# Optimization experiments

Hardware: AMD Instinct MI355X
Metric: run time of the kernel (lower is better)

## Reference

```python
import jax, jax.numpy as jnp
import numpy as np
import math

N_HEADS = 4
GROUPS = 32
EPS = 1e-5


def group_norm(x, w, b, groups=GROUPS):
    B, C, H, W = x.shape
    xg = x.reshape(B, groups, C // groups, H, W)
    mu = xg.mean(axis=(2, 3, 4), keepdims=True)
    var = xg.var(axis=(2, 3, 4), keepdims=True)
    xn = ((xg - mu) / jnp.sqrt(var + EPS)).reshape(B, C, H, W)
    return xn * w[None, :, None, None] + b[None, :, None, None]


def setup_inputs() -> dict:
    key = jax.random.key(0)
    ks = jax.random.split(key, 8)
    B, C, H, W = 4, 256, 64, 64
    s = 1.0 / math.sqrt(C)
    return {
        "x": jax.random.normal(ks[0], (B, C, H, W), jnp.float32),
        "context": jax.random.normal(ks[1], (B, C, H, W), jnp.float32),
        "gn_q_w": jnp.ones((C,), jnp.float32),
        "gn_q_b": jnp.zeros((C,), jnp.float32),
        "gn_ctx_w": jnp.ones((C,), jnp.float32),
        "gn_ctx_b": jnp.zeros((C,), jnp.float32),
        "Wq": jax.random.normal(ks[2], (C, C), jnp.float32) * s,
        "Wk": jax.random.normal(ks[3], (C, C), jnp.float32) * s,
        "Wv": jax.random.normal(ks[4], (C, C), jnp.float32) * s,
        "Wo": jax.random.normal(ks[5], (C, C), jnp.float32) * s,
        "bo": jnp.zeros((C,), jnp.float32),
    }


def reference(x, context, gn_q_w, gn_q_b, gn_ctx_w, gn_ctx_b, Wq, Wk, Wv, Wo, bo):
    B, C, H, W = x.shape
    hd = C // N_HEADS
    # 1x1 convs == channel matmuls
    q = jnp.einsum('oc,bchw->bohw', Wq, group_norm(x, gn_q_w, gn_q_b))
    k = jnp.einsum('oc,bchw->bohw', Wk, group_norm(context, gn_ctx_w, gn_ctx_b))
    v = jnp.einsum('oc,bchw->bohw', Wv, context)
    q = q.reshape(B, N_HEADS, hd, H * W)
    k = k.reshape(B, N_HEADS, hd, H * W)
    v = v.reshape(B, N_HEADS, hd, H * W)
    attn = jnp.einsum('bncd,bnce->bnde', q, k) / math.sqrt(hd)  # [B,n,HW,HW]
    attn = jax.nn.softmax(attn, axis=-1)
    out = jnp.einsum('bnde,bnce->bncd', attn, v).reshape(B, C, H, W)
    out = jnp.einsum('oc,bchw->bohw', Wo, out) + bo[None, :, None, None]
    return x + out
```

## Files before the change

kernel.cpp:

```cpp
#include <hip/hip_runtime.h>

typedef __bf16 bf16x8 __attribute__((ext_vector_type(8)));
typedef __bf16 bf16x2 __attribute__((ext_vector_type(2)));
typedef float f32x2 __attribute__((ext_vector_type(2)));
typedef float f32x4 __attribute__((ext_vector_type(4)));
typedef float f32x16 __attribute__((ext_vector_type(16)));

#define DEV static __device__ __forceinline__

DEV unsigned short f2bf(float f) {
  union { float f; unsigned int u; } v; v.f = f;
  unsigned int u = v.u;
  return (unsigned short)((u + 0x7FFFu + ((u >> 16) & 1u)) >> 16);
}

DEV float bf2f(unsigned short s) {
  union { unsigned u; float f; } v; v.u = ((unsigned)s) << 16; return v.f;
}

DEV bf16x8 ldb8(const unsigned short* p) { return *reinterpret_cast<const bf16x8*>(p); }

DEV bf16x8 ldsb8(const unsigned short* base, int byteoff) {
  return *reinterpret_cast<const bf16x8*>((const char*)base + byteoff);
}

DEV f32x4 mfma(bf16x8 a, bf16x8 b, f32x4 c) {
  return __builtin_amdgcn_mfma_f32_16x16x32_bf16(a, b, c, 0, 0, 0);
}
DEV f32x16 mfma32(bf16x8 a, bf16x8 b, f32x16 c) {
  return __builtin_amdgcn_mfma_f32_32x32x16_bf16(a, b, c, 0, 0, 0);
}

DEV float fexp2(float x) {
  float r;
  asm("v_exp_f32 %0, %1" : "=v"(r) : "v"(x));
  return r;
}

DEV unsigned cvtpk(float a, float b) {
  f32x2 t = {a, b};
  bf16x2 r = __builtin_convertvector(t, bf16x2);
  return __builtin_bit_cast(unsigned, r);
}

DEV bf16x8 pack4(unsigned w0, unsigned w1, unsigned w2, unsigned w3) {
  union { unsigned u[4]; bf16x8 v; } x;
  x.u[0] = w0; x.u[1] = w1; x.u[2] = w2; x.u[3] = w3;
  return x.v;
}

DEV f32x16 zero16() {
  f32x16 z;
#pragma unroll
  for (int i = 0; i < 16; ++i) z[i] = 0.f;
  return z;
}

__global__ __launch_bounds__(256) void gn_stats_kernel(
    const float* __restrict__ x, const float* __restrict__ ctx,
    const float* __restrict__ gqw, const float* __restrict__ gqb,
    const float* __restrict__ gcw, const float* __restrict__ gcb,
    float* __restrict__ ssbuf) {
  int id = blockIdx.x;
  int tensor = id >> 7;
  int bg = id & 127;
  int b = bg >> 5, g = bg & 31;
  const float* src = tensor ? ctx : x;
  const float* gw = tensor ? gcw : gqw;
  const float* gb = tensor ? gcb : gqb;
  float* scale = ssbuf + tensor * 2048;
  float* shift = scale + 1024;

  const float* base = src + (size_t)(b * 256 + g * 8) * 4096;
  int tid = threadIdx.x;
  float s = 0.f, sq = 0.f;
#pragma unroll
  for (int i = 0; i < 32; ++i) {
    float4 v = *reinterpret_cast<const float4*>(base + (i * 256 + tid) * 4);
    s += v.x + v.y + v.z + v.w;
    sq += v.x * v.x + v.y * v.y + v.z * v.z + v.w * v.w;
  }
#pragma unroll
  for (int sh = 32; sh; sh >>= 1) {
    s += __shfl_down(s, sh);
    sq += __shfl_down(sq, sh);
  }
  __shared__ float rs[4], rq[4], mr[2];
  int w = tid >> 6;
  if ((tid & 63) == 0) { rs[w] = s; rq[w] = sq; }
  __syncthreads();
  if (tid == 0) {
    float S = rs[0] + rs[1] + rs[2] + rs[3];
    float Q = rq[0] + rq[1] + rq[2] + rq[3];
    float mean = S * (1.f / 32768.f);
    float var = Q * (1.f / 32768.f) - mean * mean;
    mr[0] = mean;
    mr[1] = rsqrtf(var + 1e-5f);
  }
  __syncthreads();
  if (tid < 8) {
    int c = g * 8 + tid;
    float sc = gw[c] * mr[1];
    scale[b * 256 + c] = sc;
    shift[b * 256 + c] = gb[c] - mr[0] * sc;
  }
}

template <int OUTMODE>
__global__ __launch_bounds__(256) void proj_kernel(
    const float* __restrict__ W, const float* __restrict__ in,
    const float* __restrict__ scale, const float* __restrict__ shift,
    unsigned short* __restrict__ out, float wscale) {
  __shared__ unsigned short Alds[128][72];
  __shared__ unsigned short Blds[128][72];
  const int b = blockIdx.z;
  const int o0 = blockIdx.y * 128;
  const int p0 = blockIdx.x * 128;
  const int tid = threadIdx.x;
  const int w = tid >> 6, lane = tid & 63;
  const int g = lane >> 4, l15 = lane & 15;
  const int oh = (w >> 1) * 64, ph = (w & 1) * 64;

  f32x4 acc[4][4];
#pragma unroll
  for (int i = 0; i < 4; ++i)
#pragma unroll
    for (int j = 0; j < 4; ++j) acc[i][j] = (f32x4){0.f, 0.f, 0.f, 0.f};

  for (int kk = 0; kk < 4; ++kk) {
    const int c0 = kk * 64;
    __syncthreads();
#pragma unroll
    for (int i = 0; i < 8; ++i) {
      int idx = i * 256 + tid;
      int row = idx >> 4, col4 = (idx & 15) * 4;
      float4 wv = *reinterpret_cast<const float4*>(&W[(size_t)(o0 + row) * 256 + c0 + col4]);
      ushort4 bv = {f2bf(wv.x * wscale), f2bf(wv.y * wscale),
                    f2bf(wv.z * wscale), f2bf(wv.w * wscale)};
      *reinterpret_cast<ushort4*>(&Alds[row][col4]) = bv;
    }
#pragma unroll
    for (int i = 0; i < 8; ++i) {
      int idx = i * 256 + tid;
      int cc = idx >> 5, p4 = (idx & 31) * 4;
      int c = c0 + cc;
      float4 xv = *reinterpret_cast<const float4*>(&in[((size_t)b * 256 + c) * 4096 + p0 + p4]);
      float sc = 1.f, sh = 0.f;
      if (scale) { sc = scale[b * 256 + c]; sh = shift[b * 256 + c]; }
      Blds[p4 + 0][cc] = f2bf(xv.x * sc + sh);
      Blds[p4 + 1][cc] = f2bf(xv.y * sc + sh);
      Blds[p4 + 2][cc] = f2bf(xv.z * sc + sh);
      Blds[p4 + 3][cc] = f2bf(xv.w * sc + sh);
    }
    __syncthreads();
#pragma unroll
    for (int kf = 0; kf < 2; ++kf) {
      bf16x8 av[4], bv[4];
#pragma unroll
      for (int mf = 0; mf < 4; ++mf) av[mf] = ldb8(&Alds[oh + mf * 16 + l15][kf * 32 + g * 8]);
#pragma unroll
      for (int nf = 0; nf < 4; ++nf) bv[nf] = ldb8(&Blds[ph + nf * 16 + l15][kf * 32 + g * 8]);
#pragma unroll
      for (int mf = 0; mf < 4; ++mf)
#pragma unroll
        for (int nf = 0; nf < 4; ++nf) acc[mf][nf] = mfma(av[mf], bv[nf], acc[mf][nf]);
    }
  }
#pragma unroll
  for (int mf = 0; mf < 4; ++mf)
#pragma unroll
    for (int nf = 0; nf < 4; ++nf) {
      int o = o0 + oh + mf * 16 + g * 4;
      int p = p0 + ph + nf * 16 + l15;
      if (OUTMODE == 0) {
        int h = o >> 6, ch = o & 63;
        ushort4 vv = {f2bf(acc[mf][nf][0]), f2bf(acc[mf][nf][1]),
                      f2bf(acc[mf][nf][2]), f2bf(acc[mf][nf][3])};
        *reinterpret_cast<ushort4*>(&out[(((size_t)b * 4 + h) * 4096 + p) * 64 + ch]) = vv;
      } else {
#pragma unroll
        for (int r = 0; r < 4; ++r) {
          int oo = o + r;
          out[(((size_t)b * 4 + (oo >> 6)) * 64 + (oo & 63)) * 4096 + p] = f2bf(acc[mf][nf][r]);
        }
      }
    }
}

DEV void stageK32(const unsigned short* kg, int e0, char* ldsbase, int tidg) {
  int o = tidg * 16;
  int r = o >> 7;
  int col = (o & 127) ^ ((r & 7) << 4);
  const char* src = (const char*)(kg + (size_t)(e0 + r) * 64) + col;
  __builtin_amdgcn_global_load_lds(
      (__attribute__((address_space(1))) void*)src,
      (__attribute__((address_space(3))) void*)(ldsbase + (tidg >> 6) * 1024), 16, 0, 0);
}

DEV void stageV32(const unsigned short* vg, int e0, char* ldsbase, int tidg) {
  int o = tidg * 16;
  int c = o >> 6;
  int slotL = ((o >> 4) & 3) ^ ((c >> 1) & 3);
  const char* src = (const char*)(vg + (size_t)c * 4096 + e0 + slotL * 8);
  __builtin_amdgcn_global_load_lds(
      (__attribute__((address_space(1))) void*)src,
      (__attribute__((address_space(3))) void*)(ldsbase + (tidg >> 6) * 1024), 16, 0, 0);
}

__global__ __launch_bounds__(512) void attn_kernel(
    const unsigned short* __restrict__ QT, const unsigned short* __restrict__ KT,
    const unsigned short* __restrict__ V, unsigned short* __restrict__ OP,
    float* __restrict__ LP) {
  __shared__ __align__(16) char smem[34816];
  const int bh = blockIdx.x;
  const int split = blockIdx.z;
  const int tid = threadIdx.x;
  const int w = tid >> 6, lane = tid & 63;
  const int g = w >> 2, wl = w & 3;
  const int tidg = tid & 255;
  const int hi = lane >> 5, l31 = lane & 31;
  const int d = blockIdx.y * 128 + wl * 32 + l31;

  char* Kb0 = smem + g * 16384;
  char* Kb1 = Kb0 + 4096;
  char* Vb0 = Kb0 + 8192;
  char* Vb1 = Kb0 + 12288;

  const unsigned short* kg = KT + (size_t)bh * 4096 * 64;
  const unsigned short* vg = V + (size_t)bh * 64 * 4096;

  bf16x8 q[4];
#pragma unroll
  for (int ks = 0; ks < 4; ++ks)
    q[ks] = ldb8(&QT[((size_t)bh * 4096 + d) * 64 + ks * 16 + hi * 8]);

  f32x16 oacc[2];
  oacc[0] = zero16();
  oacc[1] = zero16();
  float lsum = 0.f;
  const int kswz = (l31 & 7) << 4;
  const int vswz = ((l31 >> 1) & 3) << 4;
  const int E0 = (split * 2 + g) * 1024;

  auto compute = [&](const char* kb_, const char* vb_) {
    const unsigned short* kb = (const unsigned short*)kb_;
    const unsigned short* vb = (const unsigned short*)vb_;
    f32x16 st = zero16();
    __builtin_amdgcn_s_setprio(1);
#pragma unroll
    for (int ks = 0; ks < 4; ++ks) {
      bf16x8 k0 = ldsb8(kb, l31 * 128 + ((ks * 32 + hi * 16) ^ kswz));
      st = mfma32(k0, q[ks], st);
    }
    __builtin_amdgcn_s_setprio(0);

#pragma unroll
    for (int i = 0; i < 16; ++i) st[i] = fexp2(st[i]);

    bf16x8 pf[2];
#pragma unroll
    for (int sh = 0; sh < 2; ++sh) {
      const int rb = sh * 8;
      unsigned a0 = cvtpk(st[rb + 0], st[rb + 1]);
      unsigned b0 = cvtpk(st[rb + 4], st[rb + 5]);
      unsigned a1 = cvtpk(st[rb + 2], st[rb + 3]);
      unsigned b1 = cvtpk(st[rb + 6], st[rb + 7]);
      auto r0 = __builtin_amdgcn_permlane32_swap(a0, b0, false, false);
      auto r1 = __builtin_amdgcn_permlane32_swap(a1, b1, false, false);
      pf[sh] = pack4(r0[0], r1[0], r0[1], r1[1]);
    }

    float ss[8];
#pragma unroll
    for (int i = 0; i < 8; ++i) ss[i] = st[i] + st[i + 8];
#pragma unroll
    for (int s2 = 4; s2 > 0; s2 >>= 1)
#pragma unroll
      for (int i = 0; i < s2; ++i) ss[i] += ss[i + s2];
    lsum += ss[0] + __shfl_xor(ss[0], 32);

#pragma unroll
    for (int s = 0; s < 2; ++s) {
      bf16x8 v0 = ldsb8(vb, l31 * 64 + ((s * 32 + hi * 16) ^ vswz));
      bf16x8 v1 = ldsb8(vb, (32 + l31) * 64 + ((s * 32 + hi * 16) ^ vswz));
      __builtin_amdgcn_s_setprio(1);
      oacc[0] = mfma32(v0, pf[s], oacc[0]);
      oacc[1] = mfma32(v1, pf[s], oacc[1]);
      __builtin_amdgcn_s_setprio(0);
    }
  };

  stageK32(kg, E0, Kb0, tidg);
  stageV32(vg, E0, Vb0, tidg);
  __syncthreads();

  for (int t2 = 0; t2 < 16; ++t2) {
    const int e = E0 + t2 * 64;
    stageK32(kg, e + 32, Kb1, tidg);
    stageV32(vg, e + 32, Vb1, tidg);
    compute(Kb0, Vb0);
    __syncthreads();
    if (t2 < 15) {
      stageK32(kg, e + 64, Kb0, tidg);
      stageV32(vg, e + 64, Vb0, tidg);
    }
    compute(Kb1, Vb1);
    __syncthreads();
  }

  float* combO = (float*)smem;
  float* combL = (float*)(smem + 33792);
  float* slot = combO + (wl * 64 + lane) * 33;
  if (g == 1) {
#pragma unroll
    for (int i = 0; i < 16; ++i) { slot[i] = oacc[0][i]; slot[16 + i] = oacc[1][i]; }
    combL[wl * 64 + lane] = lsum;
  }
  __syncthreads();
  if (g == 0) {
#pragma unroll
    for (int i = 0; i < 16; ++i) { oacc[0][i] += slot[i]; oacc[1][i] += slot[16 + i]; }
    lsum += combL[wl * 64 + lane];
    size_t obase = (((size_t)split * 16 + bh) * 4096 + d) * 64;
#pragma unroll
    for (int cb = 0; cb < 2; ++cb)
#pragma unroll
      for (int gq = 0; gq < 4; ++gq) {
        ushort4 sv;
        sv.x = f2bf(oacc[cb][gq * 4 + 0]);
        sv.y = f2bf(oacc[cb][gq * 4 + 1]);
        sv.z = f2bf(oacc[cb][gq * 4 + 2]);
        sv.w = f2bf(oacc[cb][gq * 4 + 3]);
        *reinterpret_cast<ushort4*>(&OP[obase + cb * 32 + gq * 8 + hi * 4]) = sv;
      }
    if (hi == 0) LP[((size_t)split * 16 + bh) * 4096 + d] = lsum;
  }
}

__global__ __launch_bounds__(256) void final_kernel(
    const float* __restrict__ Wo, const unsigned short* __restrict__ OP,
    const float* __restrict__ LP, const float* __restrict__ bo,
    const float* __restrict__ x, float* __restrict__ out) {
  __shared__ unsigned short Alds[128][72];
  __shared__ unsigned short Blds[128][72];
  const size_t OPS = (size_t)16 * 4096 * 64;
  const int b = blockIdx.z;
  const int o0 = blockIdx.y * 128;
  const int p0 = blockIdx.x * 128;
  const int tid = threadIdx.x;
  const int w = tid >> 6, lane = tid & 63;
  const int g = lane >> 4, l15 = lane & 15;
  const int oh = (w >> 1) * 64, ph = (w & 1) * 64;

  f32x4 acc[4][4];
#pragma unroll
  for (int i = 0; i < 4; ++i)
#pragma unroll
    for (int j = 0; j < 4; ++j) acc[i][j] = (f32x4){0.f, 0.f, 0.f, 0.f};

  for (int kk = 0; kk < 4; ++kk) {
    const int c0 = kk * 64;
    __syncthreads();
#pragma unroll
    for (int i = 0; i < 8; ++i) {
      int idx = i * 256 + tid;
      int row = idx >> 4, col4 = (idx & 15) * 4;
      float4 wv = *reinterpret_cast<const float4*>(&Wo[(size_t)(o0 + row) * 256 + c0 + col4]);
      ushort4 bv = {f2bf(wv.x), f2bf(wv.y), f2bf(wv.z), f2bf(wv.w)};
      *reinterpret_cast<ushort4*>(&Alds[row][col4]) = bv;
    }
#pragma unroll
    for (int i = 0; i < 4; ++i) {
      int idx = i * 256 + tid;
      int row = idx >> 3, c8 = (idx & 7) * 8;
      size_t pb = (size_t)(b * 4 + kk) * 4096 + p0 + row;
      union { uint4 u; unsigned short s[8]; } a0, a1;
      a0.u = *reinterpret_cast<const uint4*>(&OP[pb * 64 + c8]);
      a1.u = *reinterpret_cast<const uint4*>(&OP[OPS + pb * 64 + c8]);
      float ls = LP[pb] + LP[65536 + pb];
      float inv = __builtin_amdgcn_rcpf(ls);
      ushort4 r0, r1;
      r0.x = f2bf((bf2f(a0.s[0]) + bf2f(a1.s[0])) * inv);
      r0.y = f2bf((bf2f(a0.s[1]) + bf2f(a1.s[1])) * inv);
      r0.z = f2bf((bf2f(a0.s[2]) + bf2f(a1.s[2])) * inv);
      r0.w = f2bf((bf2f(a0.s[3]) + bf2f(a1.s[3])) * inv);
      r1.x = f2bf((bf2f(a0.s[4]) + bf2f(a1.s[4])) * inv);
      r1.y = f2bf((bf2f(a0.s[5]) + bf2f(a1.s[5])) * inv);
      r1.z = f2bf((bf2f(a0.s[6]) + bf2f(a1.s[6])) * inv);
      r1.w = f2bf((bf2f(a0.s[7]) + bf2f(a1.s[7])) * inv);
      *reinterpret_cast<ushort4*>(&Blds[row][c8]) = r0;
      *reinterpret_cast<ushort4*>(&Blds[row][c8 + 4]) = r1;
    }
    __syncthreads();
#pragma unroll
    for (int kf = 0; kf < 2; ++kf) {
      bf16x8 av[4], bv[4];
#pragma unroll
      for (int mf = 0; mf < 4; ++mf) av[mf] = ldb8(&Alds[oh + mf * 16 + l15][kf * 32 + g * 8]);
#pragma unroll
      for (int nf = 0; nf < 4; ++nf) bv[nf] = ldb8(&Blds[ph + nf * 16 + l15][kf * 32 + g * 8]);
#pragma unroll
      for (int mf = 0; mf < 4; ++mf)
#pragma unroll
        for (int nf = 0; nf < 4; ++nf) acc[mf][nf] = mfma(av[mf], bv[nf], acc[mf][nf]);
    }
  }
#pragma unroll
  for (int mf = 0; mf < 4; ++mf)
#pragma unroll
    for (int nf = 0; nf < 4; ++nf) {
      int o = o0 + oh + mf * 16 + g * 4;
      int p = p0 + ph + nf * 16 + l15;
#pragma unroll
      for (int r = 0; r < 4; ++r) {
        size_t idx = ((size_t)b * 256 + o + r) * 4096 + p;
        out[idx] = acc[mf][nf][r] + bo[o + r] + x[idx];
      }
    }
}

extern "C" void kernel_launch(void* const* d_in, const int* in_sizes, int n_in,
                              void* d_out, int out_size, void* d_ws, size_t ws_size,
                              hipStream_t stream) {
  const float* x = (const float*)d_in[0];
  const float* ctx = (const float*)d_in[1];
  const float* gqw = (const float*)d_in[2];
  const float* gqb = (const float*)d_in[3];
  const float* gcw = (const float*)d_in[4];
  const float* gcb = (const float*)d_in[5];
  const float* Wq = (const float*)d_in[6];
  const float* Wk = (const float*)d_in[7];
  const float* Wv = (const float*)d_in[8];
  const float* Wo = (const float*)d_in[9];
  const float* bo = (const float*)d_in[10];
  float* out = (float*)d_out;

  char* ws = (char*)d_ws;
  float* ssbuf = (float*)ws;
  float* scaleQ = ssbuf;
  float* shiftQ = ssbuf + 1024;
  float* scaleK = ssbuf + 2048;
  float* shiftK = ssbuf + 3072;
  const size_t TEN = (size_t)4 * 4 * 4096 * 64;
  unsigned short* QT = (unsigned short*)(ws + 65536);
  unsigned short* KT = QT + TEN;
  unsigned short* Vb = KT + TEN;
  unsigned short* OP = Vb + TEN;
  float* LP = (float*)(OP + 2 * TEN);

  gn_stats_kernel<<<256, 256, 0, stream>>>(x, ctx, gqw, gqb, gcw, gcb, ssbuf);

  const float beta = 0.125f * 1.44269504088896340736f;
  dim3 pg(32, 2, 4);
  proj_kernel<0><<<pg, 256, 0, stream>>>(Wq, x, scaleQ, shiftQ, QT, beta);
  proj_kernel<0><<<pg, 256, 0, stream>>>(Wk, ctx, scaleK, shiftK, KT, 1.f);
  proj_kernel<1><<<pg, 256, 0, stream>>>(Wv, ctx, nullptr, nullptr, Vb, 1.f);

  attn_kernel<<<dim3(16, 32, 2), 512, 0, stream>>>(QT, KT, Vb, OP, LP);

  final_kernel<<<pg, 256, 0, stream>>>(Wo, OP, LP, bo, x, out);
}
```

Baseline: 169.6 us.

## Merge attention key-splits into one 1024-thread block with in-LDS combine

Attention now runs its four key-range groups inside a single 1024-thread workgroup instead of two split blocks of 512. The partial outputs and row sums are reduced in shared memory in two stages, normalized, and written once as a finished bf16 output. This removes the second partial-output buffer, the row-sum buffer and the combine-and-normalize pass in the final projection. The stats, projection and final kernels also move to 1024 threads with smaller per-wave tiles. The trade-off is fewer attention blocks (512 instead of 1024), twice the LDS per block, extra barriers, and lower per-wave MFMA reuse in the GEMMs.

New measurement: 148.0 us. 1.15x faster.

```diff
diff --git a/kernel.cpp b/kernel.cpp
--- a/kernel.cpp
+++ b/kernel.cpp
@@ -14,10 +14,6 @@
   return (unsigned short)((u + 0x7FFFu + ((u >> 16) & 1u)) >> 16);
 }
 
-DEV float bf2f(unsigned short s) {
-  union { unsigned u; float f; } v; v.u = ((unsigned)s) << 16; return v.f;
-}
-
 DEV bf16x8 ldb8(const unsigned short* p) { return *reinterpret_cast<const bf16x8*>(p); }
 
 DEV bf16x8 ldsb8(const unsigned short* base, int byteoff) {
@@ -56,7 +52,7 @@
   return z;
 }
 
-__global__ __launch_bounds__(256) void gn_stats_kernel(
+__global__ __launch_bounds__(1024) void gn_stats_kernel(
     const float* __restrict__ x, const float* __restrict__ ctx,
     const float* __restrict__ gqw, const float* __restrict__ gqb,
     const float* __restrict__ gcw, const float* __restrict__ gcb,
@@ -75,8 +71,8 @@
   int tid = threadIdx.x;
   float s = 0.f, sq = 0.f;
 #pragma unroll
-  for (int i = 0; i < 32; ++i) {
-    float4 v = *reinterpret_cast<const float4*>(base + (i * 256 + tid) * 4);
+  for (int i = 0; i < 8; ++i) {
+    float4 v = *reinterpret_cast<const float4*>(base + (i * 1024 + tid) * 4);
     s += v.x + v.y + v.z + v.w;
     sq += v.x * v.x + v.y * v.y + v.z * v.z + v.w * v.w;
   }
@@ -85,13 +81,14 @@
     s += __shfl_down(s, sh);
     sq += __shfl_down(sq, sh);
   }
-  __shared__ float rs[4], rq[4], mr[2];
+  __shared__ float rs[16], rq[16], mr[2];
   int w = tid >> 6;
   if ((tid & 63) == 0) { rs[w] = s; rq[w] = sq; }
   __syncthreads();
   if (tid == 0) {
-    float S = rs[0] + rs[1] + rs[2] + rs[3];
-    float Q = rq[0] + rq[1] + rq[2] + rq[3];
+    float S = 0.f, Q = 0.f;
+#pragma unroll
+    for (int i = 0; i < 16; ++i) { S += rs[i]; Q += rq[i]; }
     float mean = S * (1.f / 32768.f);
     float var = Q * (1.f / 32768.f) - mean * mean;
     mr[0] = mean;
@@ -107,7 +104,7 @@
 }
 
 template <int OUTMODE>
-__global__ __launch_bounds__(256) void proj_kernel(
+__global__ __launch_bounds__(1024) void proj_kernel(
     const float* __restrict__ W, const float* __restrict__ in,
     const float* __restrict__ scale, const float* __restrict__ shift,
     unsigned short* __restrict__ out, float wscale) {
@@ -119,20 +116,20 @@
   const int tid = threadIdx.x;
   const int w = tid >> 6, lane = tid & 63;
   const int g = lane >> 4, l15 = lane & 15;
-  const int oh = (w >> 1) * 64, ph = (w & 1) * 64;
-
-  f32x4 acc[4][4];
-#pragma unroll
-  for (int i = 0; i < 4; ++i)
-#pragma unroll
-    for (int j = 0; j < 4; ++j) acc[i][j] = (f32x4){0.f, 0.f, 0.f, 0.f};
+  const int oh = (w >> 2) * 32, ph = (w & 3) * 32;
+
+  f32x4 acc[2][2];
+#pragma unroll
+  for (int i = 0; i < 2; ++i)
+#pragma unroll
+    for (int j = 0; j < 2; ++j) acc[i][j] = (f32x4){0.f, 0.f, 0.f, 0.f};
 
   for (int kk = 0; kk < 4; ++kk) {
     const int c0 = kk * 64;
     __syncthreads();
 #pragma unroll
-    for (int i = 0; i < 8; ++i) {
-      int idx = i * 256 + tid;
+    for (int i = 0; i < 2; ++i) {
+      int idx = i * 1024 + tid;
       int row = idx >> 4, col4 = (idx & 15) * 4;
       float4 wv = *reinterpret_cast<const float4*>(&W[(size_t)(o0 + row) * 256 + c0 + col4]);
       ushort4 bv = {f2bf(wv.x * wscale), f2bf(wv.y * wscale),
@@ -140,8 +137,8 @@
       *reinterpret_cast<ushort4*>(&Alds[row][col4]) = bv;
     }
 #pragma unroll
-    for (int i = 0; i < 8; ++i) {
-      int idx = i * 256 + tid;
+    for (int i = 0; i < 2; ++i) {
+      int idx = i * 1024 + tid;
       int cc = idx >> 5, p4 = (idx & 31) * 4;
       int c = c0 + cc;
       float4 xv = *reinterpret_cast<const float4*>(&in[((size_t)b * 256 + c) * 4096 + p0 + p4]);
@@ -155,21 +152,21 @@
     __syncthreads();
 #pragma unroll
     for (int kf = 0; kf < 2; ++kf) {
-      bf16x8 av[4], bv[4];
-#pragma unroll
-      for (int mf = 0; mf < 4; ++mf) av[mf] = ldb8(&Alds[oh + mf * 16 + l15][kf * 32 + g * 8]);
-#pragma unroll
-      for (int nf = 0; nf < 4; ++nf) bv[nf] = ldb8(&Blds[ph + nf * 16 + l15][kf * 32 + g * 8]);
-#pragma unroll
-      for (int mf = 0; mf < 4; ++mf)
-#pragma unroll
-        for (int nf = 0; nf < 4; ++nf) acc[mf][nf] = mfma(av[mf], bv[nf], acc[mf][nf]);
-    }
-  }
-#pragma unroll
-  for (int mf = 0; mf < 4; ++mf)
-#pragma unroll
-    for (int nf = 0; nf < 4; ++nf) {
+      bf16x8 av[2], bv[2];
+#pragma unroll
+      for (int mf = 0; mf < 2; ++mf) av[mf] = ldb8(&Alds[oh + mf * 16 + l15][kf * 32 + g * 8]);
+#pragma unroll
+      for (int nf = 0; nf < 2; ++nf) bv[nf] = ldb8(&Blds[ph + nf * 16 + l15][kf * 32 + g * 8]);
+#pragma unroll
+      for (int mf = 0; mf < 2; ++mf)
+#pragma unroll
+        for (int nf = 0; nf < 2; ++nf) acc[mf][nf] = mfma(av[mf], bv[nf], acc[mf][nf]);
+    }
+  }
+#pragma unroll
+  for (int mf = 0; mf < 2; ++mf)
+#pragma unroll
+    for (int nf = 0; nf < 2; ++nf) {
       int o = o0 + oh + mf * 16 + g * 4;
       int p = p0 + ph + nf * 16 + l15;
       if (OUTMODE == 0) {
@@ -207,13 +204,11 @@
       (__attribute__((address_space(3))) void*)(ldsbase + (tidg >> 6) * 1024), 16, 0, 0);
 }
 
-__global__ __launch_bounds__(512) void attn_kernel(
+__global__ __launch_bounds__(1024) void attn_kernel(
     const unsigned short* __restrict__ QT, const unsigned short* __restrict__ KT,
-    const unsigned short* __restrict__ V, unsigned short* __restrict__ OP,
-    float* __restrict__ LP) {
-  __shared__ __align__(16) char smem[34816];
+    const unsigned short* __restrict__ V, unsigned short* __restrict__ OT) {
+  __shared__ __align__(16) char smem[67584];
   const int bh = blockIdx.x;
-  const int split = blockIdx.z;
   const int tid = threadIdx.x;
   const int w = tid >> 6, lane = tid & 63;
   const int g = w >> 2, wl = w & 3;
@@ -240,7 +235,7 @@
   float lsum = 0.f;
   const int kswz = (l31 & 7) << 4;
   const int vswz = ((l31 >> 1) & 3) << 4;
-  const int E0 = (split * 2 + g) * 1024;
+  const int E0 = g * 1024;
 
   auto compute = [&](const char* kb_, const char* vb_) {
     const unsigned short* kb = (const unsigned short*)kb_;
@@ -308,107 +303,108 @@
     __syncthreads();
   }
 
-  float* combO = (float*)smem;
-  float* combL = (float*)(smem + 33792);
-  float* slot = combO + (wl * 64 + lane) * 33;
-  if (g == 1) {
-#pragma unroll
-    for (int i = 0; i < 16; ++i) { slot[i] = oacc[0][i]; slot[16 + i] = oacc[1][i]; }
-    combL[wl * 64 + lane] = lsum;
+  float* slab = (float*)smem;
+  float* myA = slab + (wl * 64 + lane) * 33;
+  float* myB = myA + 256 * 33;
+  if (g == 1 || g == 3) {
+    float* p = (g == 1) ? myA : myB;
+#pragma unroll
+    for (int i = 0; i < 16; ++i) { p[i] = oacc[0][i]; p[16 + i] = oacc[1][i]; }
+    p[32] = lsum;
   }
   __syncthreads();
   if (g == 0) {
 #pragma unroll
-    for (int i = 0; i < 16; ++i) { oacc[0][i] += slot[i]; oacc[1][i] += slot[16 + i]; }
-    lsum += combL[wl * 64 + lane];
-    size_t obase = (((size_t)split * 16 + bh) * 4096 + d) * 64;
+    for (int i = 0; i < 16; ++i) { oacc[0][i] += myA[i]; oacc[1][i] += myA[16 + i]; }
+    lsum += myA[32];
+  }
+  if (g == 2) {
+#pragma unroll
+    for (int i = 0; i < 16; ++i) { oacc[0][i] += myB[i]; oacc[1][i] += myB[16 + i]; }
+    lsum += myB[32];
+  }
+  __syncthreads();
+  if (g == 2) {
+#pragma unroll
+    for (int i = 0; i < 16; ++i) { myA[i] = oacc[0][i]; myA[16 + i] = oacc[1][i]; }
+    myA[32] = lsum;
+  }
+  __syncthreads();
+  if (g == 0) {
+#pragma unroll
+    for (int i = 0; i < 16; ++i) { oacc[0][i] += myA[i]; oacc[1][i] += myA[16 + i]; }
+    lsum += myA[32];
+    float inv = 1.f / lsum;
+    size_t obase = ((size_t)bh * 4096 + d) * 64;
 #pragma unroll
     for (int cb = 0; cb < 2; ++cb)
 #pragma unroll
       for (int gq = 0; gq < 4; ++gq) {
         ushort4 sv;
-        sv.x = f2bf(oacc[cb][gq * 4 + 0]);
-        sv.y = f2bf(oacc[cb][gq * 4 + 1]);
-        sv.z = f2bf(oacc[cb][gq * 4 + 2]);
-        sv.w = f2bf(oacc[cb][gq * 4 + 3]);
-        *reinterpret_cast<ushort4*>(&OP[obase + cb * 32 + gq * 8 + hi * 4]) = sv;
+        sv.x = f2bf(oacc[cb][gq * 4 + 0] * inv);
+        sv.y = f2bf(oacc[cb][gq * 4 + 1] * inv);
+        sv.z = f2bf(oacc[cb][gq * 4 + 2] * inv);
+        sv.w = f2bf(oacc[cb][gq * 4 + 3] * inv);
+        *reinterpret_cast<ushort4*>(&OT[obase + cb * 32 + gq * 8 + hi * 4]) = sv;
       }
-    if (hi == 0) LP[((size_t)split * 16 + bh) * 4096 + d] = lsum;
-  }
-}
-
-__global__ __launch_bounds__(256) void final_kernel(
-    const float* __restrict__ Wo, const unsigned short* __restrict__ OP,
-    const float* __restrict__ LP, const float* __restrict__ bo,
-    const float* __restrict__ x, float* __restrict__ out) {
+  }
+}
+
+__global__ __launch_bounds__(1024) void final_kernel(
+    const float* __restrict__ Wo, const unsigned short* __restrict__ OT,
+    const float* __restrict__ bo, const float* __restrict__ x,
+    float* __restrict__ out) {
   __shared__ unsigned short Alds[128][72];
   __shared__ unsigned short Blds[128][72];
-  const size_t OPS = (size_t)16 * 4096 * 64;
   const int b = blockIdx.z;
   const int o0 = blockIdx.y * 128;
   const int p0 = blockIdx.x * 128;
   const int tid = threadIdx.x;
   const int w = tid >> 6, lane = tid & 63;
   const int g = lane >> 4, l15 = lane & 15;
-  const int oh = (w >> 1) * 64, ph = (w & 1) * 64;
-
-  f32x4 acc[4][4];
-#pragma unroll
-  for (int i = 0; i < 4; ++i)
-#pragma unroll
-    for (int j = 0; j < 4; ++j) acc[i][j] = (f32x4){0.f, 0.f, 0.f, 0.f};
+  const int oh = (w >> 2) * 32, ph = (w & 3) * 32;
+
+  f32x4 acc[2][2];
+#pragma unroll
+  for (int i = 0; i < 2; ++i)
+#pragma unroll
+    for (int j = 0; j < 2; ++j) acc[i][j] = (f32x4){0.f, 0.f, 0.f, 0.f};
 
   for (int kk = 0; kk < 4; ++kk) {
     const int c0 = kk * 64;
     __syncthreads();
 #pragma unroll
-    for (int i = 0; i < 8; ++i) {
-      int idx = i * 256 + tid;
+    for (int i = 0; i < 2; ++i) {
+      int idx = i * 1024 + tid;
       int row = idx >> 4, col4 = (idx & 15) * 4;
       float4 wv = *reinterpret_cast<const float4*>(&Wo[(size_t)(o0 + row) * 256 + c0 + col4]);
       ushort4 bv = {f2bf(wv.x), f2bf(wv.y), f2bf(wv.z), f2bf(wv.w)};
       *reinterpret_cast<ushort4*>(&Alds[row][col4]) = bv;
     }
-#pragma unroll
-    for (int i = 0; i < 4; ++i) {
-      int idx = i * 256 + tid;
+    {
+      int idx = tid;
       int row = idx >> 3, c8 = (idx & 7) * 8;
-      size_t pb = (size_t)(b * 4 + kk) * 4096 + p0 + row;
-      union { uint4 u; unsigned short s[8]; } a0, a1;
-      a0.u = *reinterpret_cast<const uint4*>(&OP[pb * 64 + c8]);
-      a1.u = *reinterpret_cast<const uint4*>(&OP[OPS + pb * 64 + c8]);
-      float ls = LP[pb] + LP[65536 + pb];
-      float inv = __builtin_amdgcn_rcpf(ls);
-      ushort4 r0, r1;
-      r0.x = f2bf((bf2f(a0.s[0]) + bf2f(a1.s[0])) * inv);
-      r0.y = f2bf((bf2f(a0.s[1]) + bf2f(a1.s[1])) * inv);
-      r0.z = f2bf((bf2f(a0.s[2]) + bf2f(a1.s[2])) * inv);
-      r0.w = f2bf((bf2f(a0.s[3]) + bf2f(a1.s[3])) * inv);
-      r1.x = f2bf((bf2f(a0.s[4]) + bf2f(a1.s[4])) * inv);
-      r1.y = f2bf((bf2f(a0.s[5]) + bf2f(a1.s[5])) * inv);
-      r1.z = f2bf((bf2f(a0.s[6]) + bf2f(a1.s[6])) * inv);
-      r1.w = f2bf((bf2f(a0.s[7]) + bf2f(a1.s[7])) * inv);
-      *reinterpret_cast<ushort4*>(&Blds[row][c8]) = r0;
-      *reinterpret_cast<ushort4*>(&Blds[row][c8 + 4]) = r1;
+      *reinterpret_cast<uint4*>(&Blds[row][c8]) =
+          *reinterpret_cast<const uint4*>(&OT[(((size_t)b * 4 + kk) * 4096 + p0 + row) * 64 + c8]);
     }
     __syncthreads();
 #pragma unroll
     for (int kf = 0; kf < 2; ++kf) {
-      bf16x8 av[4], bv[4];
-#pragma unroll
-      for (int mf = 0; mf < 4; ++mf) av[mf] = ldb8(&Alds[oh + mf * 16 + l15][kf * 32 + g * 8]);
-#pragma unroll
-      for (int nf = 0; nf < 4; ++nf) bv[nf] = ldb8(&Blds[ph + nf * 16 + l15][kf * 32 + g * 8]);
-#pragma unroll
-      for (int mf = 0; mf < 4; ++mf)
-#pragma unroll
-        for (int nf = 0; nf < 4; ++nf) acc[mf][nf] = mfma(av[mf], bv[nf], acc[mf][nf]);
-    }
-  }
-#pragma unroll
-  for (int mf = 0; mf < 4; ++mf)
-#pragma unroll
-    for (int nf = 0; nf < 4; ++nf) {
+      bf16x8 av[2], bv[2];
+#pragma unroll
+      for (int mf = 0; mf < 2; ++mf) av[mf] = ldb8(&Alds[oh + mf * 16 + l15][kf * 32 + g * 8]);
+#pragma unroll
+      for (int nf = 0; nf < 2; ++nf) bv[nf] = ldb8(&Blds[ph + nf * 16 + l15][kf * 32 + g * 8]);
+#pragma unroll
+      for (int mf = 0; mf < 2; ++mf)
+#pragma unroll
+        for (int nf = 0; nf < 2; ++nf) acc[mf][nf] = mfma(av[mf], bv[nf], acc[mf][nf]);
+    }
+  }
+#pragma unroll
+  for (int mf = 0; mf < 2; ++mf)
+#pragma unroll
+    for (int nf = 0; nf < 2; ++nf) {
       int o = o0 + oh + mf * 16 + g * 4;
       int p = p0 + ph + nf * 16 + l15;
 #pragma unroll
@@ -445,18 +441,17 @@
   unsigned short* QT = (unsigned short*)(ws + 65536);
   unsigned short* KT = QT + TEN;
   unsigned short* Vb = KT + TEN;
-  unsigned short* OP = Vb + TEN;
-  float* LP = (float*)(OP + 2 * TEN);
-
-  gn_stats_kernel<<<256, 256, 0, stream>>>(x, ctx, gqw, gqb, gcw, gcb, ssbuf);
+  unsigned short* OT = Vb + TEN;
+
+  gn_stats_kernel<<<256, 1024, 0, stream>>>(x, ctx, gqw, gqb, gcw, gcb, ssbuf);
 
   const float beta = 0.125f * 1.44269504088896340736f;
   dim3 pg(32, 2, 4);
-  proj_kernel<0><<<pg, 256, 0, stream>>>(Wq, x, scaleQ, shiftQ, QT, beta);
-  proj_kernel<0><<<pg, 256, 0, stream>>>(Wk, ctx, scaleK, shiftK, KT, 1.f);
-  proj_kernel<1><<<pg, 256, 0, stream>>>(Wv, ctx, nullptr, nullptr, Vb, 1.f);
-
-  attn_kernel<<<dim3(16, 32, 2), 512, 0, stream>>>(QT, KT, Vb, OP, LP);
-
-  final_kernel<<<pg, 256, 0, stream>>>(Wo, OP, LP, bo, x, out);
-}
+  proj_kernel<0><<<pg, 1024, 0, stream>>>(Wq, x, scaleQ, shiftQ, QT, beta);
+  proj_kernel<0><<<pg, 1024, 0, stream>>>(Wk, ctx, scaleK, shiftK, KT, 1.f);
+  proj_kernel<1><<<pg, 1024, 0, stream>>>(Wv, ctx, nullptr, nullptr, Vb, 1.f);
+
+  attn_kernel<<<dim3(16, 32), 1024, 0, stream>>>(QT, KT, Vb, OT);
+
+  final_kernel<<<pg, 1024, 0, stream>>>(Wo, OT, bo, x, out);
+}
```
